# Optimization experiments

Hardware: AMD Instinct MI355X
Metric: run time of the kernel (lower is better)

The kernel has to match this reference:

```python
import jax, jax.numpy as jnp
import numpy as np

N, E = 20000, 320000
NFEAT, NHID = 512, 1024
DROPOUT_P = 0.5


def setup_inputs() -> dict:
    key = jax.random.key(0)
    ks = jax.random.split(key, 9)
    x = jax.random.normal(ks[0], (N, NFEAT), dtype=jnp.float32)
    W1 = jax.random.normal(ks[1], (NFEAT, NHID), dtype=jnp.float32) / np.sqrt(NFEAT)
    b1 = jnp.zeros((NHID,), dtype=jnp.float32)
    W2 = jax.random.normal(ks[2], (NHID, NFEAT), dtype=jnp.float32) / np.sqrt(NHID)
    b2 = jnp.zeros((NFEAT,), dtype=jnp.float32)
    adj_vals = jax.random.uniform(ks[3], (E,), dtype=jnp.float32)
    u_drop = jax.random.uniform(ks[4], (N, NHID), dtype=jnp.float32)
    src = jax.random.randint(ks[5], (E,), 0, N, dtype=jnp.int64)
    dst = jax.random.randint(ks[6], (E,), 0, N, dtype=jnp.int64)
    return {"x": x, "W1": W1, "b1": b1, "W2": W2, "b2": b2,
            "adj_vals": adj_vals, "u_drop": u_drop, "src": src, "dst": dst}


def _graph_conv(h, W, b, adj_vals, src, dst, n_nodes):
    # GraphConvolution: adj @ (h @ W) + b, with adj in COO form (src, dst, vals)
    support = h @ W                                   # [N, d_out]
    msgs = adj_vals[:, None] * support[src]           # [E, d_out]
    agg = jax.ops.segment_sum(msgs, dst, num_segments=n_nodes)
    return agg + b


def reference(x, W1, b1, W2, b2, adj_vals, u_drop, src, dst):
    h = jax.nn.relu(_graph_conv(x, W1, b1, adj_vals, src, dst, N))
    # inverted dropout (training=True), deterministic via u_drop
    keep = (u_drop > DROPOUT_P).astype(h.dtype) / (1.0 - DROPOUT_P)
    h = h * keep
    out = _graph_conv(h, W2, b2, adj_vals, src, dst, N)
    return out
```

## Files before the change

### kernel.cpp

```cpp
#include <hip/hip_runtime.h>
#include <hip/hip_bf16.h>

typedef __attribute__((ext_vector_type(8))) short short8;
typedef __attribute__((ext_vector_type(4))) float f32x4;

#define N_NODES 20000
#define N_EDGES 320000
#define NFEAT 512
#define NHID 1024
#define MBTOT 1252

__device__ __forceinline__ float bf2f(unsigned short u) {
    union { unsigned int i; float f; } c; c.i = ((unsigned int)u) << 16; return c.f;
}
__device__ __forceinline__ unsigned short f2bf(float f) {
    union { float f; unsigned int i; } c; c.f = f;
    unsigned int x = c.i;
    return (unsigned short)((x + 0x7fffu + ((x >> 16) & 1u)) >> 16);
}


__global__ void hist_kernel(const int* __restrict__ dst, int* __restrict__ deg, int E) {
    int e = blockIdx.x * 256 + threadIdx.x;
    if (e < E) atomicAdd(&deg[dst[e]], 1);
}

__global__ __launch_bounds__(1024) void scan_kernel(const int* __restrict__ deg,
                                                    int* __restrict__ row_ptr,
                                                    int* __restrict__ cursor, int n) {
    __shared__ int sdata[1024];
    const int t = threadIdx.x;
    constexpr int CH = 20;
    int base = t * CH;
    int local[CH];
    int sum = 0;
#pragma unroll
    for (int i = 0; i < CH; ++i) {
        int idx = base + i;
        int v = (idx < n) ? deg[idx] : 0;
        local[i] = sum;
        sum += v;
    }
    sdata[t] = sum;
    __syncthreads();
    for (int off = 1; off < 1024; off <<= 1) {
        int v = (t >= off) ? sdata[t - off] : 0;
        __syncthreads();
        sdata[t] += v;
        __syncthreads();
    }
    int prev = (t == 0) ? 0 : sdata[t - 1];
#pragma unroll
    for (int i = 0; i < CH; ++i) {
        int idx = base + i;
        if (idx < n) {
            int p = prev + local[i];
            row_ptr[idx] = p;
            cursor[idx]  = p;
        }
    }
    if (t == 1023) row_ptr[n] = sdata[1023];
}

__global__ void fill_kernel(const int* __restrict__ src, const int* __restrict__ dst,
                            const float* __restrict__ vals, int* __restrict__ cursor,
                            int* __restrict__ csr_off, float* __restrict__ csr_val, int E) {
    int e = blockIdx.x * 256 + threadIdx.x;
    if (e < E) {
        int d = dst[e];
        int pos = atomicAdd(&cursor[d], 1);
        csr_off[pos] = src[e] << 10;
        csr_val[pos] = vals[e];
    }
}


__global__ void transpose_cvt_pk(const float* __restrict__ W, unsigned short* __restrict__ Bp,
                                 int K, int N) {
    __shared__ float tile[32][33];
    const int KT = K >> 5;
    int ntx = N >> 5;
    int k0 = (blockIdx.x / ntx) << 5;
    int n0 = (blockIdx.x % ntx) << 5;
    int tx = threadIdx.x & 31, ty = threadIdx.x >> 5;
#pragma unroll
    for (int i = 0; i < 32; i += 8)
        tile[ty + i][tx] = W[(size_t)(k0 + ty + i) * N + n0 + tx];
    __syncthreads();
#pragma unroll
    for (int i = 0; i < 32; i += 8) {
        int n = n0 + ty + i;
        int k = k0 + tx;
        int nb = n >> 4, rl = n & 15;
        int kb = k >> 5, kq = (k & 31) >> 3, j = k & 7;
        Bp[((((size_t)nb * KT + kb) * 64) + kq * 16 + rl) * 8 + j] = f2bf(tile[tx][ty + i]);
    }
}


__global__ void cvt_bf16_kernel(const float* __restrict__ x, unsigned short* __restrict__ xb,
                                int n8) {
    int i = blockIdx.x * 256 + threadIdx.x;
    if (i < n8) {
        f32x4 v0 = ((const f32x4*)x)[i * 2];
        f32x4 v1 = ((const f32x4*)x)[i * 2 + 1];
        short8 o;
#pragma unroll
        for (int j = 0; j < 4; ++j) {
            o[j]     = (short)f2bf(v0[j]);
            o[4 + j] = (short)f2bf(v1[j]);
        }
        ((short8*)xb)[i] = o;
    }
}


__global__ __launch_bounds__(256) void mask_kernel(const float* __restrict__ u,
                                                   unsigned int* __restrict__ mask) {
    __shared__ unsigned char nib[256];
    size_t base = (size_t)blockIdx.x * 2048;
    int t = threadIdx.x;
    f32x4 v0 = ((const f32x4*)(u + base))[t * 2];
    f32x4 v1 = ((const f32x4*)(u + base))[t * 2 + 1];
    unsigned n = 0;
#pragma unroll
    for (int j = 0; j < 4; ++j) {
        n |= (v0[j] > 0.5f ? 1u : 0u) << j;
        n |= (v1[j] > 0.5f ? 1u : 0u) << (4 + j);
    }
    nib[t] = (unsigned char)n;
    __syncthreads();
    if (t < 64) {
        unsigned w = (unsigned)nib[t * 4] | ((unsigned)nib[t * 4 + 1] << 8) |
                     ((unsigned)nib[t * 4 + 2] << 16) | ((unsigned)nib[t * 4 + 3] << 24);
        mask[base / 32 + t] = w;
    }
}


__global__ __launch_bounds__(256) void agg1_kernel(const unsigned short* __restrict__ xbf,
                                                   const int* __restrict__ csr_off,
                                                   const float* __restrict__ csr_val,
                                                   const int* __restrict__ row_ptr,
                                                   unsigned short* __restrict__ A1p) {
    const int c = blockIdx.x & 7;
    const int dbase = (blockIdx.x >> 3) * 32;
    const int wid = threadIdx.x >> 6;
    const int lane = threadIdx.x & 63;
    const int g = lane >> 3;
    const int s = lane & 7;
    const int d = dbase + wid * 8 + g;
    const int e0 = row_ptr[d], e1 = row_ptr[d + 1];
    const char* xc = (const char*)xbf + (c * 64 + s * 8) * 2;

    f32x4 a0 = {0.f, 0.f, 0.f, 0.f}, a1 = {0.f, 0.f, 0.f, 0.f};
    const int glane = g * 8;

    for (int eb = e0; eb < e1; eb += 8) {
        int cnt = e1 - eb; if (cnt > 8) cnt = 8;
        int ov = 0; float fv = 0.f;
        if (s < cnt) { ov = csr_off[eb + s]; fv = csr_val[eb + s]; }
        if (cnt == 8) {
#pragma unroll
            for (int i = 0; i < 8; ++i) {
                int off = __shfl(ov, glane + i);
                float val = __shfl(fv, glane + i);
                short8 w = *(const short8*)(xc + off);
#pragma unroll
                for (int j = 0; j < 4; ++j) {
                    a0[j] += val * bf2f((unsigned short)w[j]);
                    a1[j] += val * bf2f((unsigned short)w[4 + j]);
                }
            }
        } else {
            for (int i = 0; i < cnt; ++i) {
                int off = __shfl(ov, glane + i);
                float val = __shfl(fv, glane + i);
                short8 w = *(const short8*)(xc + off);
#pragma unroll
                for (int j = 0; j < 4; ++j) {
                    a0[j] += val * bf2f((unsigned short)w[j]);
                    a1[j] += val * bf2f((unsigned short)w[4 + j]);
                }
            }
        }
    }
    short8 o;
#pragma unroll
    for (int j = 0; j < 4; ++j) {
        o[j]     = (short)f2bf(a0[j]);
        o[4 + j] = (short)f2bf(a1[j]);
    }
    size_t idx = ((((size_t)(d >> 4) * (NFEAT / 32) + (c * 2 + (s >> 2))) * 64) +
                  (s & 3) * 16 + (d & 15)) * 8;
    *(short8*)&A1p[idx] = o;
}


__global__ __launch_bounds__(256) void agg2_kernel(const unsigned short* __restrict__ s2,
                                                   const int* __restrict__ csr_off,
                                                   const float* __restrict__ csr_val,
                                                   const int* __restrict__ row_ptr,
                                                   const float* __restrict__ b2,
                                                   float* __restrict__ out) {
    const int c = blockIdx.x & 7;
    const int dbase = (blockIdx.x >> 3) * 32;
    const int wid = threadIdx.x >> 6;
    const int lane = threadIdx.x & 63;
    const int g = lane >> 3;
    const int s = lane & 7;
    const int d = dbase + wid * 8 + g;
    const int e0 = row_ptr[d], e1 = row_ptr[d + 1];
    const int fb = c * 64 + s * 8;
    const char* xc = (const char*)s2 + fb * 2;

    f32x4 a0 = *(const f32x4*)&b2[fb];
    f32x4 a1 = *(const f32x4*)&b2[fb + 4];
    const int glane = g * 8;

    for (int eb = e0; eb < e1; eb += 8) {
        int cnt = e1 - eb; if (cnt > 8) cnt = 8;
        int ov = 0; float fv = 0.f;
        if (s < cnt) { ov = csr_off[eb + s]; fv = csr_val[eb + s]; }
        if (cnt == 8) {
#pragma unroll
            for (int i = 0; i < 8; ++i) {
                int off = __shfl(ov, glane + i);
                float val = __shfl(fv, glane + i);
                short8 w = *(const short8*)(xc + off);
#pragma unroll
                for (int j = 0; j < 4; ++j) {
                    a0[j] += val * bf2f((unsigned short)w[j]);
                    a1[j] += val * bf2f((unsigned short)w[4 + j]);
                }
            }
        } else {
            for (int i = 0; i < cnt; ++i) {
                int off = __shfl(ov, glane + i);
                float val = __shfl(fv, glane + i);
                short8 w = *(const short8*)(xc + off);
#pragma unroll
                for (int j = 0; j < 4; ++j) {
                    a0[j] += val * bf2f((unsigned short)w[j]);
                    a1[j] += val * bf2f((unsigned short)w[4 + j]);
                }
            }
        }
    }
    *(f32x4*)&out[(size_t)d * NFEAT + fb]     = a0;
    *(f32x4*)&out[(size_t)d * NFEAT + fb + 4] = a1;
}


template <int EPI, int KT, int NW>
__global__ __launch_bounds__(256, 4) void gemm_pk(
    const unsigned short* __restrict__ Ap,
    const unsigned short* __restrict__ Bp,
    unsigned short* __restrict__ C,
    int M,
    const float* __restrict__ bias,
    const unsigned int* __restrict__ umask) {
    constexpr int N = NW * 64;
    constexpr int MI_MAX = 625;

    const int nwg = gridDim.x;
    const int bid = blockIdx.x;
    const int q = nwg >> 3, r = nwg & 7;
    const int xcd = bid & 7, pos = bid >> 3;
    const int swz = (xcd < r ? xcd * (q + 1) : r * (q + 1) + (xcd - r) * q) + pos;

    const int wid = threadIdx.x >> 6;
    const int lane = threadIdx.x & 63;
    const int rl = lane & 15;
    const int kq = lane >> 4;

    constexpr int NT2 = NW / 2;
    const int bm = swz / NT2;
    const int bn = swz % NT2;
    int mi = bm * 2 + (wid >> 1); if (mi >= MI_MAX) mi = MI_MAX - 1;
    const int ni = bn * 2 + (wid & 1);

    const unsigned short* ab = Ap + (size_t)(mi * 2) * KT * 512 + lane * 8;
    const unsigned short* bb = Bp + (size_t)(ni * 4) * KT * 512 + lane * 8;

    f32x4 acc[2][4] = {};
    short8 aX[2], bX[4], aY[2], bY[4];

#pragma unroll
    for (int m = 0; m < 2; ++m) aX[m] = *(const short8*)(ab + (size_t)m * KT * 512);
#pragma unroll
    for (int n = 0; n < 4; ++n) bX[n] = *(const short8*)(bb + (size_t)n * KT * 512);

#pragma unroll 1
    for (int kb = 0; kb < KT; kb += 2) {
#pragma unroll
        for (int m = 0; m < 2; ++m)
            aY[m] = *(const short8*)(ab + ((size_t)m * KT + kb + 1) * 512);
#pragma unroll
        for (int n = 0; n < 4; ++n)
            bY[n] = *(const short8*)(bb + ((size_t)n * KT + kb + 1) * 512);
#pragma unroll
        for (int m = 0; m < 2; ++m)
#pragma unroll
            for (int n = 0; n < 4; ++n)
                acc[m][n] = __builtin_amdgcn_mfma_f32_16x16x32_bf16(aX[m], bX[n], acc[m][n], 0, 0, 0);
        if (kb + 2 < KT) {
#pragma unroll
            for (int m = 0; m < 2; ++m)
                aX[m] = *(const short8*)(ab + ((size_t)m * KT + kb + 2) * 512);
#pragma unroll
            for (int n = 0; n < 4; ++n)
                bX[n] = *(const short8*)(bb + ((size_t)n * KT + kb + 2) * 512);
        }
#pragma unroll
        for (int m = 0; m < 2; ++m)
#pragma unroll
            for (int n = 0; n < 4; ++n)
                acc[m][n] = __builtin_amdgcn_mfma_f32_16x16x32_bf16(aY[m], bY[n], acc[m][n], 0, 0, 0);
    }

    if constexpr (EPI == 1) {
        __shared__ unsigned short ltr[4][32][40];
        constexpr int KT2 = N / 32;
#pragma unroll
        for (int n2 = 0; n2 < 2; ++n2) {
#pragma unroll
            for (int m = 0; m < 2; ++m) {
#pragma unroll
                for (int nn = 0; nn < 2; ++nn) {
                    int n = n2 * 2 + nn;
                    float bv = bias[ni * 64 + n * 16 + rl];
#pragma unroll
                    for (int j = 0; j < 4; ++j) {
                        float v = acc[m][n][j] + bv;
                        v = v > 0.f ? v : 0.f;
                        ltr[wid][m * 16 + kq * 4 + j][nn * 16 + rl] = f2bf(v);
                    }
                }
            }
            __builtin_amdgcn_s_waitcnt(0);
#pragma unroll
            for (int m2 = 0; m2 < 2; ++m2) {
                int row = m2 * 16 + rl;
                int gr = mi * 32 + row;
                unsigned w = umask[(size_t)gr * (N >> 5) + (ni * 2 + n2)];
                short8 u = *(const short8*)&ltr[wid][row][kq * 8];
                short8 o;
#pragma unroll
                for (int j = 0; j < 4; ++j) {
                    o[j]     = ((w >> (kq * 8 + j)) & 1u)
                               ? (short)f2bf(bf2f((unsigned short)u[j]) * 2.0f) : (short)0;
                    o[4 + j] = ((w >> (kq * 8 + 4 + j)) & 1u)
                               ? (short)f2bf(bf2f((unsigned short)u[4 + j]) * 2.0f) : (short)0;
                }
                int mbg = mi * 2 + m2;
                size_t dst = (((size_t)mbg * KT2 + (ni * 2 + n2)) * 64 + lane) * 8;
                *(short8*)&C[dst] = o;
            }
            __builtin_amdgcn_s_waitcnt(0);
        }
    } else {
        const int crow = kq * 4;
#pragma unroll
        for (int m = 0; m < 2; ++m) {
#pragma unroll
            for (int n = 0; n < 4; ++n) {
                int gr0 = mi * 32 + m * 16 + crow;
                int gc = ni * 64 + n * 16 + rl;
#pragma unroll
                for (int j = 0; j < 4; ++j) {
                    int gr = gr0 + j;
                    if (gr < M)
                        C[(size_t)gr * N + gc] = f2bf(acc[m][n][j]);
                }
            }
        }
    }
}


extern "C" void kernel_launch(void* const* d_in, const int* in_sizes, int n_in,
                              void* d_out, int out_size, void* d_ws, size_t ws_size,
                              hipStream_t stream) {
    const float* x        = (const float*)d_in[0];
    const float* W1       = (const float*)d_in[1];
    const float* b1       = (const float*)d_in[2];
    const float* W2       = (const float*)d_in[3];
    const float* b2       = (const float*)d_in[4];
    const float* adj_vals = (const float*)d_in[5];
    const float* u_drop   = (const float*)d_in[6];
    const int*   src      = (const int*)d_in[7];
    const int*   dst      = (const int*)d_in[8];
    float* out = (float*)d_out;

    char* p = (char*)d_ws;
    auto take = [&](size_t bytes) {
        char* q = p;
        p += (bytes + 255) & ~(size_t)255;
        return q;
    };
    int* deg        = (int*)take((size_t)N_NODES * 4);
    int* row_ptr    = (int*)take((size_t)(N_NODES + 1) * 4);
    int* cursor     = (int*)take((size_t)N_NODES * 4);
    int* csr_off    = (int*)take((size_t)N_EDGES * 4);
    float* csr_val  = (float*)take((size_t)N_EDGES * 4);
    unsigned short* w1p   = (unsigned short*)take((size_t)NFEAT * NHID * 2);
    unsigned short* w2p   = (unsigned short*)take((size_t)NFEAT * NHID * 2);
    unsigned short* xbf   = (unsigned short*)take((size_t)N_NODES * NFEAT * 2);
    unsigned short* a1p   = (unsigned short*)take((size_t)MBTOT * (NFEAT / 32) * 1024);
    unsigned short* a2p   = (unsigned short*)take((size_t)MBTOT * (NHID / 32) * 1024);
    unsigned short* s2buf = (unsigned short*)take((size_t)N_NODES * NFEAT * 2);
    unsigned int* umask   = (unsigned int*)take((size_t)N_NODES * (NHID / 32) * 4);

    hipMemsetAsync(deg, 0, (size_t)N_NODES * 4, stream);
    hist_kernel<<<(N_EDGES + 255) / 256, 256, 0, stream>>>(dst, deg, N_EDGES);
    scan_kernel<<<1, 1024, 0, stream>>>(deg, row_ptr, cursor, N_NODES);
    fill_kernel<<<(N_EDGES + 255) / 256, 256, 0, stream>>>(src, dst, adj_vals, cursor,
                                                           csr_off, csr_val, N_EDGES);
    transpose_cvt_pk<<<(NFEAT / 32) * (NHID / 32), 256, 0, stream>>>(W1, w1p, NFEAT, NHID);
    transpose_cvt_pk<<<(NHID / 32) * (NFEAT / 32), 256, 0, stream>>>(W2, w2p, NHID, NFEAT);
    cvt_bf16_kernel<<<(N_NODES * NFEAT / 8 + 255) / 256, 256, 0, stream>>>(
        x, xbf, N_NODES * NFEAT / 8);
    mask_kernel<<<N_NODES * NHID / 2048, 256, 0, stream>>>(u_drop, umask);

    agg1_kernel<<<8 * 625, 256, 0, stream>>>(xbf, csr_off, csr_val, row_ptr, a1p);

    gemm_pk<1, NFEAT / 32, NHID / 64><<<313 * (NHID / 128), 256, 0, stream>>>(
        a1p, w1p, a2p, N_NODES, b1, umask);
    gemm_pk<0, NHID / 32, NFEAT / 64><<<313 * (NFEAT / 128), 256, 0, stream>>>(
        a2p, w2p, s2buf, N_NODES, nullptr, nullptr);

    agg2_kernel<<<8 * 625, 256, 0, stream>>>(s2buf, csr_off, csr_val, row_ptr, b2, out);
}
```

Measured before the change: 258.7 us.

## Pack CSR entries, prefetch edges in aggregation, merge prep kernels, parallelize scan

Replaces the single-block scan with a three-stage multi-block scan and packs CSR offsets and values into one int2 array. The two transposes are merged into one launch, as are the bf16 conversion and dropout mask. The aggregation kernels prefetch the next edge batch and issue all eight gathers before accumulating, to increase memory-level parallelism. This adds register pressure in the aggregation kernels and more scan launches.

```diff
diff --git a/kernel.cpp b/kernel.cpp
--- a/kernel.cpp
+++ b/kernel.cpp
@@ -9,6 +9,7 @@
 #define NFEAT 512
 #define NHID 1024
 #define MBTOT 1252
+#define SCAN_NB 79
 
 __device__ __forceinline__ float bf2f(unsigned short u) {
     union { unsigned int i; float f; } c; c.i = ((unsigned int)u) << 16; return c.f;
@@ -25,63 +26,76 @@
     if (e < E) atomicAdd(&deg[dst[e]], 1);
 }
 
-__global__ __launch_bounds__(1024) void scan_kernel(const int* __restrict__ deg,
-                                                    int* __restrict__ row_ptr,
-                                                    int* __restrict__ cursor, int n) {
-    __shared__ int sdata[1024];
-    const int t = threadIdx.x;
-    constexpr int CH = 20;
-    int base = t * CH;
-    int local[CH];
-    int sum = 0;
-#pragma unroll
-    for (int i = 0; i < CH; ++i) {
-        int idx = base + i;
-        int v = (idx < n) ? deg[idx] : 0;
-        local[i] = sum;
-        sum += v;
-    }
-    sdata[t] = sum;
+__global__ __launch_bounds__(256) void scan_a(const int* __restrict__ deg,
+                                              int* __restrict__ rp,
+                                              int* __restrict__ part, int n) {
+    __shared__ int sd[256];
+    int t = threadIdx.x;
+    int i = blockIdx.x * 256 + t;
+    int v = (i < n) ? deg[i] : 0;
+    int acc = v;
+    sd[t] = acc;
     __syncthreads();
-    for (int off = 1; off < 1024; off <<= 1) {
-        int v = (t >= off) ? sdata[t - off] : 0;
+    for (int off = 1; off < 256; off <<= 1) {
+        int u = (t >= off) ? sd[t - off] : 0;
         __syncthreads();
-        sdata[t] += v;
+        acc += u;
+        sd[t] = acc;
         __syncthreads();
     }
-    int prev = (t == 0) ? 0 : sdata[t - 1];
-#pragma unroll
-    for (int i = 0; i < CH; ++i) {
-        int idx = base + i;
-        if (idx < n) {
-            int p = prev + local[i];
-            row_ptr[idx] = p;
-            cursor[idx]  = p;
-        }
-    }
-    if (t == 1023) row_ptr[n] = sdata[1023];
+    if (i < n) rp[i] = acc - v;
+    if (t == 255) part[blockIdx.x] = acc;
+}
+
+__global__ __launch_bounds__(256) void scan_b(int* __restrict__ part, int nb) {
+    __shared__ int sd[256];
+    int t = threadIdx.x;
+    int v = (t < nb) ? part[t] : 0;
+    int acc = v;
+    sd[t] = acc;
+    __syncthreads();
+    for (int off = 1; off < 256; off <<= 1) {
+        int u = (t >= off) ? sd[t - off] : 0;
+        __syncthreads();
+        acc += u;
+        sd[t] = acc;
+        __syncthreads();
+    }
+    if (t < nb) part[t] = acc - v;
+    if (t == 255) part[nb] = acc;
+}
+
+__global__ __launch_bounds__(256) void scan_c(int* __restrict__ rp, int* __restrict__ cursor,
+                                              const int* __restrict__ part, int n, int nb) {
+    int i = blockIdx.x * 256 + threadIdx.x;
+    if (i < n) {
+        int v = rp[i] + part[blockIdx.x];
+        rp[i] = v;
+        cursor[i] = v;
+    }
+    if (i == 0) rp[n] = part[nb];
 }
 
 __global__ void fill_kernel(const int* __restrict__ src, const int* __restrict__ dst,
                             const float* __restrict__ vals, int* __restrict__ cursor,
-                            int* __restrict__ csr_off, float* __restrict__ csr_val, int E) {
+                            int2* __restrict__ csr_ov, int E) {
     int e = blockIdx.x * 256 + threadIdx.x;
     if (e < E) {
         int d = dst[e];
         int pos = atomicAdd(&cursor[d], 1);
-        csr_off[pos] = src[e] << 10;
-        csr_val[pos] = vals[e];
-    }
-}
-
-
-__global__ void transpose_cvt_pk(const float* __restrict__ W, unsigned short* __restrict__ Bp,
-                                 int K, int N) {
+        csr_ov[pos] = make_int2(src[e] << 10, __float_as_int(vals[e]));
+    }
+}
+
+
+__device__ __forceinline__ void transpose_body(const float* __restrict__ W,
+                                               unsigned short* __restrict__ Bp,
+                                               int K, int N, int bid) {
     __shared__ float tile[32][33];
     const int KT = K >> 5;
     int ntx = N >> 5;
-    int k0 = (blockIdx.x / ntx) << 5;
-    int n0 = (blockIdx.x % ntx) << 5;
+    int k0 = (bid / ntx) << 5;
+    int n0 = (bid % ntx) << 5;
     int tx = threadIdx.x & 31, ty = threadIdx.x >> 5;
 #pragma unroll
     for (int i = 0; i < 32; i += 8)
@@ -97,11 +111,24 @@
     }
 }
 
-
-__global__ void cvt_bf16_kernel(const float* __restrict__ x, unsigned short* __restrict__ xb,
-                                int n8) {
-    int i = blockIdx.x * 256 + threadIdx.x;
-    if (i < n8) {
+__global__ __launch_bounds__(256) void transpose2_kernel(const float* __restrict__ W1,
+                                                         unsigned short* __restrict__ w1p,
+                                                         const float* __restrict__ W2,
+                                                         unsigned short* __restrict__ w2p) {
+    if (blockIdx.x < 512) transpose_body(W1, w1p, NFEAT, NHID, blockIdx.x);
+    else                  transpose_body(W2, w2p, NHID, NFEAT, blockIdx.x - 512);
+}
+
+
+__global__ __launch_bounds__(256) void prep_kernel(const float* __restrict__ x,
+                                                   unsigned short* __restrict__ xb,
+                                                   const float* __restrict__ u,
+                                                   unsigned int* __restrict__ mask) {
+    __shared__ unsigned char nib[256];
+    int b = blockIdx.x;
+    int t = threadIdx.x;
+    if (b < 5000) {
+        int i = b * 256 + t;
         f32x4 v0 = ((const f32x4*)x)[i * 2];
         f32x4 v1 = ((const f32x4*)x)[i * 2 + 1];
         short8 o;
@@ -111,36 +138,29 @@
             o[4 + j] = (short)f2bf(v1[j]);
         }
         ((short8*)xb)[i] = o;
-    }
-}
-
-
-__global__ __launch_bounds__(256) void mask_kernel(const float* __restrict__ u,
-                                                   unsigned int* __restrict__ mask) {
-    __shared__ unsigned char nib[256];
-    size_t base = (size_t)blockIdx.x * 2048;
-    int t = threadIdx.x;
-    f32x4 v0 = ((const f32x4*)(u + base))[t * 2];
-    f32x4 v1 = ((const f32x4*)(u + base))[t * 2 + 1];
-    unsigned n = 0;
-#pragma unroll
-    for (int j = 0; j < 4; ++j) {
-        n |= (v0[j] > 0.5f ? 1u : 0u) << j;
-        n |= (v1[j] > 0.5f ? 1u : 0u) << (4 + j);
-    }
-    nib[t] = (unsigned char)n;
-    __syncthreads();
-    if (t < 64) {
-        unsigned w = (unsigned)nib[t * 4] | ((unsigned)nib[t * 4 + 1] << 8) |
-                     ((unsigned)nib[t * 4 + 2] << 16) | ((unsigned)nib[t * 4 + 3] << 24);
-        mask[base / 32 + t] = w;
+    } else {
+        size_t base = (size_t)(b - 5000) * 2048;
+        f32x4 v0 = ((const f32x4*)(u + base))[t * 2];
+        f32x4 v1 = ((const f32x4*)(u + base))[t * 2 + 1];
+        unsigned n = 0;
+#pragma unroll
+        for (int j = 0; j < 4; ++j) {
+            n |= (v0[j] > 0.5f ? 1u : 0u) << j;
+            n |= (v1[j] > 0.5f ? 1u : 0u) << (4 + j);
+        }
+        nib[t] = (unsigned char)n;
+        __syncthreads();
+        if (t < 64) {
+            unsigned w = (unsigned)nib[t * 4] | ((unsigned)nib[t * 4 + 1] << 8) |
+                         ((unsigned)nib[t * 4 + 2] << 16) | ((unsigned)nib[t * 4 + 3] << 24);
+            mask[base / 32 + t] = w;
+        }
     }
 }
 
 
 __global__ __launch_bounds__(256) void agg1_kernel(const unsigned short* __restrict__ xbf,
-                                                   const int* __restrict__ csr_off,
-                                                   const float* __restrict__ csr_val,
+                                                   const int2* __restrict__ csr_ov,
                                                    const int* __restrict__ row_ptr,
                                                    unsigned short* __restrict__ A1p) {
     const int c = blockIdx.x & 7;
@@ -152,19 +172,35 @@
     const int d = dbase + wid * 8 + g;
     const int e0 = row_ptr[d], e1 = row_ptr[d + 1];
     const char* xc = (const char*)xbf + (c * 64 + s * 8) * 2;
+    const int glane = g * 8;
 
     f32x4 a0 = {0.f, 0.f, 0.f, 0.f}, a1 = {0.f, 0.f, 0.f, 0.f};
-    const int glane = g * 8;
+
+    int offX = 0; float valX = 0.f;
+    if (e0 + s < e1) { int2 t = csr_ov[e0 + s]; offX = t.x; valX = __int_as_float(t.y); }
 
     for (int eb = e0; eb < e1; eb += 8) {
+        int offY = 0; float valY = 0.f;
+        if (eb + 8 + s < e1) { int2 t = csr_ov[eb + 8 + s]; offY = t.x; valY = __int_as_float(t.y); }
         int cnt = e1 - eb; if (cnt > 8) cnt = 8;
-        int ov = 0; float fv = 0.f;
-        if (s < cnt) { ov = csr_off[eb + s]; fv = csr_val[eb + s]; }
         if (cnt == 8) {
+            short8 w[8];
+#pragma unroll
+            for (int i = 0; i < 8; ++i)
+                w[i] = *(const short8*)(xc + __shfl(offX, glane + i));
 #pragma unroll
             for (int i = 0; i < 8; ++i) {
-                int off = __shfl(ov, glane + i);
-                float val = __shfl(fv, glane + i);
+                float val = __shfl(valX, glane + i);
+#pragma unroll
+                for (int j = 0; j < 4; ++j) {
+                    a0[j] += val * bf2f((unsigned short)w[i][j]);
+                    a1[j] += val * bf2f((unsigned short)w[i][4 + j]);
+                }
+            }
+        } else {
+            for (int i = 0; i < cnt; ++i) {
+                int off = __shfl(offX, glane + i);
+                float val = __shfl(valX, glane + i);
                 short8 w = *(const short8*)(xc + off);
 #pragma unroll
                 for (int j = 0; j < 4; ++j) {
@@ -172,18 +208,8 @@
                     a1[j] += val * bf2f((unsigned short)w[4 + j]);
                 }
             }
-        } else {
-            for (int i = 0; i < cnt; ++i) {
-                int off = __shfl(ov, glane + i);
-                float val = __shfl(fv, glane + i);
-                short8 w = *(const short8*)(xc + off);
-#pragma unroll
-                for (int j = 0; j < 4; ++j) {
-                    a0[j] += val * bf2f((unsigned short)w[j]);
-                    a1[j] += val * bf2f((unsigned short)w[4 + j]);
-                }
-            }
-        }
+        }
+        offX = offY; valX = valY;
     }
     short8 o;
 #pragma unroll
@@ -198,8 +224,7 @@
 
 
 __global__ __launch_bounds__(256) void agg2_kernel(const unsigned short* __restrict__ s2,
-                                                   const int* __restrict__ csr_off,
-                                                   const float* __restrict__ csr_val,
+                                                   const int2* __restrict__ csr_ov,
                                                    const int* __restrict__ row_ptr,
                                                    const float* __restrict__ b2,
                                                    float* __restrict__ out) {
@@ -213,20 +238,36 @@
     const int e0 = row_ptr[d], e1 = row_ptr[d + 1];
     const int fb = c * 64 + s * 8;
     const char* xc = (const char*)s2 + fb * 2;
+    const int glane = g * 8;
 
     f32x4 a0 = *(const f32x4*)&b2[fb];
     f32x4 a1 = *(const f32x4*)&b2[fb + 4];
-    const int glane = g * 8;
+
+    int offX = 0; float valX = 0.f;
+    if (e0 + s < e1) { int2 t = csr_ov[e0 + s]; offX = t.x; valX = __int_as_float(t.y); }
 
     for (int eb = e0; eb < e1; eb += 8) {
+        int offY = 0; float valY = 0.f;
+        if (eb + 8 + s < e1) { int2 t = csr_ov[eb + 8 + s]; offY = t.x; valY = __int_as_float(t.y); }
         int cnt = e1 - eb; if (cnt > 8) cnt = 8;
-        int ov = 0; float fv = 0.f;
-        if (s < cnt) { ov = csr_off[eb + s]; fv = csr_val[eb + s]; }
         if (cnt == 8) {
+            short8 w[8];
+#pragma unroll
+            for (int i = 0; i < 8; ++i)
+                w[i] = *(const short8*)(xc + __shfl(offX, glane + i));
 #pragma unroll
             for (int i = 0; i < 8; ++i) {
-                int off = __shfl(ov, glane + i);
-                float val = __shfl(fv, glane + i);
+                float val = __shfl(valX, glane + i);
+#pragma unroll
+                for (int j = 0; j < 4; ++j) {
+                    a0[j] += val * bf2f((unsigned short)w[i][j]);
+                    a1[j] += val * bf2f((unsigned short)w[i][4 + j]);
+                }
+            }
+        } else {
+            for (int i = 0; i < cnt; ++i) {
+                int off = __shfl(offX, glane + i);
+                float val = __shfl(valX, glane + i);
                 short8 w = *(const short8*)(xc + off);
 #pragma unroll
                 for (int j = 0; j < 4; ++j) {
@@ -234,18 +275,8 @@
                     a1[j] += val * bf2f((unsigned short)w[4 + j]);
                 }
             }
-        } else {
-            for (int i = 0; i < cnt; ++i) {
-                int off = __shfl(ov, glane + i);
-                float val = __shfl(fv, glane + i);
-                short8 w = *(const short8*)(xc + off);
-#pragma unroll
-                for (int j = 0; j < 4; ++j) {
-                    a0[j] += val * bf2f((unsigned short)w[j]);
-                    a1[j] += val * bf2f((unsigned short)w[4 + j]);
-                }
-            }
-        }
+        }
+        offX = offY; valX = valY;
     }
     *(f32x4*)&out[(size_t)d * NFEAT + fb]     = a0;
     *(f32x4*)&out[(size_t)d * NFEAT + fb + 4] = a1;
@@ -402,8 +433,8 @@
     int* deg        = (int*)take((size_t)N_NODES * 4);
     int* row_ptr    = (int*)take((size_t)(N_NODES + 1) * 4);
     int* cursor     = (int*)take((size_t)N_NODES * 4);
-    int* csr_off    = (int*)take((size_t)N_EDGES * 4);
-    float* csr_val  = (float*)take((size_t)N_EDGES * 4);
+    int* part       = (int*)take((size_t)(SCAN_NB + 1) * 4);
+    int2* csr_ov    = (int2*)take((size_t)N_EDGES * 8);
     unsigned short* w1p   = (unsigned short*)take((size_t)NFEAT * NHID * 2);
     unsigned short* w2p   = (unsigned short*)take((size_t)NFEAT * NHID * 2);
     unsigned short* xbf   = (unsigned short*)take((size_t)N_NODES * NFEAT * 2);
@@ -414,21 +445,20 @@
 
     hipMemsetAsync(deg, 0, (size_t)N_NODES * 4, stream);
     hist_kernel<<<(N_EDGES + 255) / 256, 256, 0, stream>>>(dst, deg, N_EDGES);
-    scan_kernel<<<1, 1024, 0, stream>>>(deg, row_ptr, cursor, N_NODES);
+    scan_a<<<SCAN_NB, 256, 0, stream>>>(deg, row_ptr, part, N_NODES);
+    scan_b<<<1, 256, 0, stream>>>(part, SCAN_NB);
+    scan_c<<<SCAN_NB, 256, 0, stream>>>(row_ptr, cursor, part, N_NODES, SCAN_NB);
     fill_kernel<<<(N_EDGES + 255) / 256, 256, 0, stream>>>(src, dst, adj_vals, cursor,
-                                                           csr_off, csr_val, N_EDGES);
-    transpose_cvt_pk<<<(NFEAT / 32) * (NHID / 32), 256, 0, stream>>>(W1, w1p, NFEAT, NHID);
-    transpose_cvt_pk<<<(NHID / 32) * (NFEAT / 32), 256, 0, stream>>>(W2, w2p, NHID, NFEAT);
-    cvt_bf16_kernel<<<(N_NODES * NFEAT / 8 + 255) / 256, 256, 0, stream>>>(
-        x, xbf, N_NODES * NFEAT / 8);
-    mask_kernel<<<N_NODES * NHID / 2048, 256, 0, stream>>>(u_drop, umask);
-
-    agg1_kernel<<<8 * 625, 256, 0, stream>>>(xbf, csr_off, csr_val, row_ptr, a1p);
+                                                           csr_ov, N_EDGES);
+    transpose2_kernel<<<1024, 256, 0, stream>>>(W1, w1p, W2, w2p);
+    prep_kernel<<<15000, 256, 0, stream>>>(x, xbf, u_drop, umask);
+
+    agg1_kernel<<<8 * 625, 256, 0, stream>>>(xbf, csr_ov, row_ptr, a1p);
 
     gemm_pk<1, NFEAT / 32, NHID / 64><<<313 * (NHID / 128), 256, 0, stream>>>(
         a1p, w1p, a2p, N_NODES, b1, umask);
     gemm_pk<0, NHID / 32, NFEAT / 64><<<313 * (NFEAT / 128), 256, 0, stream>>>(
         a2p, w2p, s2buf, N_NODES, nullptr, nullptr);
 
-    agg2_kernel<<<8 * 625, 256, 0, stream>>>(s2buf, csr_off, csr_val, row_ptr, b2, out);
-}
+    agg2_kernel<<<8 * 625, 256, 0, stream>>>(s2buf, csr_ov, row_ptr, b2, out);
+}
```

Result: faster. 232.0 us (-10.3%).
